# Kernel tuning notes

Hardware: AMD Instinct MI355X
Metric: run time of the kernel (lower is better)

The kernel has to match this reference:

```python
import jax, jax.numpy as jnp
import numpy as np
import math

B, W, D_IN, H = 64, 512, 300, 512

def setup_inputs() -> dict:
    key = jax.random.key(0)
    ks = jax.random.split(key, 8)
    s = 1.0 / math.sqrt(D_IN)
    return {
        "char_vectors": jax.random.normal(ks[0], (B, W, D_IN), jnp.float32),
        "word_vectors": jax.random.normal(ks[1], (B, W, D_IN), jnp.float32),
        "Wk": jax.random.uniform(ks[2], (D_IN, H), jnp.float32, -s, s),
        "bk": jnp.zeros((H,), jnp.float32),
        "Wq": jax.random.uniform(ks[3], (D_IN, H), jnp.float32, -s, s),
        "bq": jnp.zeros((H,), jnp.float32),
        "Wv": jax.random.uniform(ks[4], (D_IN, H), jnp.float32, -s, s),
        "bv": jnp.zeros((H,), jnp.float32),
    }

def reference(char_vectors, word_vectors, Wk, bk, Wq, bq, Wv, bv):
    # Stack word/char reps per word -> [B, W, 2, H]
    def proj(Wm, bm):
        return jnp.stack([word_vectors @ Wm + bm, char_vectors @ Wm + bm], axis=2)
    K = proj(Wk, bk)
    Q = proj(Wq, bq)
    V = proj(Wv, bv)
    temp = jnp.sqrt(jnp.asarray(H, jnp.float32))
    # tiny 2x2 attention per word, fully batched (dropout off = eval mode)
    attn = jnp.einsum("bwqh,bwkh->bwqk", Q, K) / temp
    attn = jax.nn.softmax(attn, axis=-1)
    out = jnp.einsum("bwqk,bwkh->bwqh", attn, V)  # [B, W, 2, H]
    return out.reshape(B, W, 2 * H)
```

## Files before the change

### kernel.cpp

```cpp
#include <hip/hip_runtime.h>

#define D 300
#define KP 328
#define KSTEPS 10
#define WPB 64
#define ROWS 128
#define NSEG 41
#define CHUNK_BYTES 41984

typedef __attribute__((ext_vector_type(4))) float f32x4;
typedef __attribute__((ext_vector_type(8))) short bf16x8;

__device__ inline unsigned short f2bf(float f) {
  unsigned int u = __float_as_uint(f);
  unsigned int r = (u + 0x7fffu + ((u >> 16) & 1u)) >> 16;
  return (unsigned short)r;
}

__device__ inline void gload_lds16(const void* g, void* l) {
  __builtin_amdgcn_global_load_lds(
      (const __attribute__((address_space(1))) unsigned int*)g,
      (__attribute__((address_space(3))) unsigned int*)l, 16, 0, 0);
}

__global__ __launch_bounds__(512) void prep_weights(
    const float* __restrict__ Wq, const float* __restrict__ Wk,
    const float* __restrict__ Wv, unsigned short* __restrict__ wt) {
  int idx = blockIdx.x * 512 + threadIdx.x;
  if (idx >= 1536 * KP) return;
  int n = idx / KP, k = idx - n * KP;
  const float* src = (n < 512) ? Wq : ((n < 1024) ? Wk : Wv);
  int col = n & 511;
  float v = (k < D) ? src[k * 512 + col] : 0.0f;
  wt[idx] = f2bf(v);
}

__device__ __forceinline__ void proj_chunk(
    const unsigned short* __restrict__ bufp, const float* __restrict__ biasL,
    int nbase, int cg, int lrow, int kgrp,
    const bf16x8 (&a)[2][KSTEPS], f32x4 (&acc)[2][2]) {
#pragma unroll
  for (int rt = 0; rt < 2; ++rt)
#pragma unroll
    for (int ct = 0; ct < 2; ++ct) {
      float b = biasL[nbase + cg * 32 + ct * 16 + lrow];
      acc[rt][ct] = (f32x4){b, b, b, b};
    }
#pragma unroll
  for (int ks = 0; ks < KSTEPS; ++ks) {
    const unsigned short* bp = bufp + cg * 32 * KP + ks * 32 + kgrp * 8;
    bf16x8 b0 = *(const bf16x8*)(bp + lrow * KP);
    bf16x8 b1 = *(const bf16x8*)(bp + (16 + lrow) * KP);
    acc[0][0] = __builtin_amdgcn_mfma_f32_16x16x32_bf16(a[0][ks], b0, acc[0][0], 0, 0, 0);
    acc[1][0] = __builtin_amdgcn_mfma_f32_16x16x32_bf16(a[1][ks], b0, acc[1][0], 0, 0, 0);
    acc[0][1] = __builtin_amdgcn_mfma_f32_16x16x32_bf16(a[0][ks], b1, acc[0][1], 0, 0, 0);
    acc[1][1] = __builtin_amdgcn_mfma_f32_16x16x32_bf16(a[1][ks], b1, acc[1][1], 0, 0, 0);
  }
}

__global__ __launch_bounds__(512, 2) void fused_attn(
    const float* __restrict__ charv, const float* __restrict__ wordv,
    const unsigned short* __restrict__ wt,
    const float* __restrict__ bk, const float* __restrict__ bq,
    const float* __restrict__ bv, float* __restrict__ out) {
  extern __shared__ char lds[];
  float* biasL = (float*)(lds + 2 * CHUNK_BYTES);
  float* sS    = biasL + 1536;
  float* sAt   = sS + 512;

  const int tid  = threadIdx.x;
  const int wid  = tid >> 6;
  const int lane = tid & 63;
  const int lrow = lane & 15;
  const int kgrp = lane >> 4;
  const int rg   = wid >> 1;
  const int cg   = wid & 1;

  auto chunk_n = [](int t) {
    return (t < 16) ? ((t & 1) * 512 + (t >> 1) * 64) : (1024 + (t - 16) * 64);
  };
  auto stage = [&](int t) {
    const char* src = (const char*)(wt + chunk_n(t) * KP);
    char* dst = lds + (t & 1) * CHUNK_BYTES;
    for (int j = wid; j < NSEG; j += 8)
      gload_lds16(src + j * 1024 + lane * 16, dst + j * 1024);
  };

  stage(0);
  for (int i = tid; i < 1536; i += 512) {
    float v = (i < 512) ? bq[i] : ((i < 1024) ? bk[i - 512] : bv[i - 1024]);
    biasL[i] = v;
  }

  bf16x8 a[2][KSTEPS];
#pragma unroll
  for (int rt = 0; rt < 2; ++rt) {
    int row = blockIdx.x * ROWS + rg * 32 + rt * 16 + lrow;
    const float* rp = ((row & 1) ? charv : wordv) + (row >> 1) * D;
#pragma unroll
    for (int ks = 0; ks < KSTEPS; ++ks) {
      int k0 = ks * 32 + kgrp * 8;
      float4 lo = {0.f, 0.f, 0.f, 0.f}, hi = {0.f, 0.f, 0.f, 0.f};
      if (k0 + 8 <= D) {
        lo = *(const float4*)(rp + k0);
        hi = *(const float4*)(rp + k0 + 4);
      } else if (k0 < D) {
        lo = *(const float4*)(rp + k0);
      }
      bf16x8 v;
      v[0] = (short)f2bf(lo.x); v[1] = (short)f2bf(lo.y);
      v[2] = (short)f2bf(lo.z); v[3] = (short)f2bf(lo.w);
      v[4] = (short)f2bf(hi.x); v[5] = (short)f2bf(hi.y);
      v[6] = (short)f2bf(hi.z); v[7] = (short)f2bf(hi.w);
      a[rt][ks] = v;
    }
  }
  __syncthreads();

  float p[2][8];
#pragma unroll
  for (int rt = 0; rt < 2; ++rt)
#pragma unroll
    for (int t = 0; t < 8; ++t) p[rt][t] = 0.f;

  int tg = 0;
  for (int g = 0; g < 8; ++g) {
    f32x4 accQ[2][2], accK[2][2];

    stage(tg + 1);
    proj_chunk((const unsigned short*)(lds + (tg & 1) * CHUNK_BYTES), biasL,
               g * 64, cg, lrow, kgrp, a, accQ);
    __syncthreads(); ++tg;

    stage(tg + 1);
    proj_chunk((const unsigned short*)(lds + (tg & 1) * CHUNK_BYTES), biasL,
               512 + g * 64, cg, lrow, kgrp, a, accK);
#pragma unroll
    for (int rt = 0; rt < 2; ++rt)
#pragma unroll
      for (int ct = 0; ct < 2; ++ct)
#pragma unroll
        for (int wl = 0; wl < 2; ++wl)
#pragma unroll
          for (int i = 0; i < 2; ++i)
#pragma unroll
            for (int j = 0; j < 2; ++j)
              p[rt][wl * 4 + i * 2 + j] += accQ[rt][ct][wl * 2 + i] * accK[rt][ct][wl * 2 + j];
    __syncthreads(); ++tg;
  }

#pragma unroll
  for (int rt = 0; rt < 2; ++rt)
#pragma unroll
    for (int t = 0; t < 8; ++t) {
      float v = p[rt][t];
      v += __shfl_xor(v, 1);
      v += __shfl_xor(v, 2);
      v += __shfl_xor(v, 4);
      v += __shfl_xor(v, 8);
      p[rt][t] = v;
    }
  if (lrow == 0) {
#pragma unroll
    for (int rt = 0; rt < 2; ++rt)
#pragma unroll
      for (int t = 0; t < 8; ++t) {
        int w = rg * 16 + rt * 8 + kgrp * 2 + (t >> 2);
        sS[cg * 256 + w * 4 + (t & 3)] = p[rt][t];
      }
  }
  __syncthreads();
  if (tid < 64) {
    const float sc = 0.044194173824159216f;
    float s[4];
#pragma unroll
    for (int t = 0; t < 4; ++t) s[t] = (sS[tid * 4 + t] + sS[256 + tid * 4 + t]) * sc;
#pragma unroll
    for (int i = 0; i < 2; ++i) {
      float m  = fmaxf(s[i * 2], s[i * 2 + 1]);
      float e0 = expf(s[i * 2] - m), e1 = expf(s[i * 2 + 1] - m);
      float inv = 1.0f / (e0 + e1);
      sAt[tid * 4 + i * 2]     = e0 * inv;
      sAt[tid * 4 + i * 2 + 1] = e1 * inv;
    }
  }
  __syncthreads();

  float at0[2][4], at1[2][4];
#pragma unroll
  for (int rt = 0; rt < 2; ++rt) {
    int wA = rg * 16 + rt * 8 + kgrp * 2;
#pragma unroll
    for (int t = 0; t < 4; ++t) {
      at0[rt][t] = sAt[wA * 4 + t];
      at1[rt][t] = sAt[(wA + 1) * 4 + t];
    }
  }

  for (int g = 0; g < 8; ++g) {
    if (tg + 1 < 24) stage(tg + 1);
    f32x4 accV[2][2];
    proj_chunk((const unsigned short*)(lds + (tg & 1) * CHUNK_BYTES), biasL,
               1024 + g * 64, cg, lrow, kgrp, a, accV);

#pragma unroll
    for (int rt = 0; rt < 2; ++rt) {
      int wA = rg * 16 + rt * 8 + kgrp * 2;
      int gA = blockIdx.x * WPB + wA;
#pragma unroll
      for (int ct = 0; ct < 2; ++ct) {
        int h = g * 64 + cg * 32 + ct * 16 + lrow;
        float* o = out + gA * 1024 + h;
        o[0]    = at0[rt][0] * accV[rt][ct][0] + at0[rt][1] * accV[rt][ct][1];
        o[512]  = at0[rt][2] * accV[rt][ct][0] + at0[rt][3] * accV[rt][ct][1];
        o[1024] = at1[rt][0] * accV[rt][ct][2] + at1[rt][1] * accV[rt][ct][3];
        o[1536] = at1[rt][2] * accV[rt][ct][2] + at1[rt][3] * accV[rt][ct][3];
      }
    }
    if (g < 7) __syncthreads();
    ++tg;
  }
}

extern "C" void kernel_launch(void* const* d_in, const int* in_sizes, int n_in,
                              void* d_out, int out_size, void* d_ws, size_t ws_size,
                              hipStream_t stream) {
  const float* charv = (const float*)d_in[0];
  const float* wordv = (const float*)d_in[1];
  const float* Wk = (const float*)d_in[2];
  const float* bk = (const float*)d_in[3];
  const float* Wq = (const float*)d_in[4];
  const float* bq = (const float*)d_in[5];
  const float* Wv = (const float*)d_in[6];
  const float* bv = (const float*)d_in[7];
  float* out = (float*)d_out;
  unsigned short* wt = (unsigned short*)d_ws;

  prep_weights<<<(1536 * KP + 511) / 512, 512, 0, stream>>>(Wq, Wk, Wv, wt);

  const int lds_bytes = 2 * CHUNK_BYTES + 1536 * 4 + 512 * 4 + 256 * 4;
  fused_attn<<<32768 / WPB, 512, lds_bytes, stream>>>(charv, wordv, wt, bk, bq, bv, out);
}
```

Before: 98.16 us.

## Double rows per block and interleave Q/K halves into one staged chunk

Each block now handles 256 rows (128 words) instead of 128, so every staged weight chunk in LDS is reused across four row tiles per wave. That halves total weight traffic from L2 and the barrier count per row. The Q/K phase now stages 32 Q columns and their matching 32 K columns together in one chunk, cutting that phase to 16 pipelined steps with no Q-then-K barrier in between. The A-fragment registers double to 4x10 bf16x8, which raises VGPR pressure under launch_bounds(512,2). The grid drops to 256 blocks, which may underfill the GPU's CUs.

Measured after the change: 126.0 us. +28.4%, slower.

```diff
diff --git a/kernel.cpp b/kernel.cpp
--- a/kernel.cpp
+++ b/kernel.cpp
@@ -3,10 +3,12 @@
 #define D 300
 #define KP 328
 #define KSTEPS 10
-#define WPB 64
-#define ROWS 128
+#define WPB 128
+#define ROWS 256
 #define NSEG 41
 #define CHUNK_BYTES 41984
+#define HALF_BYTES 20992
+#define NCHUNK 24
 
 typedef __attribute__((ext_vector_type(4))) float f32x4;
 typedef __attribute__((ext_vector_type(8))) short bf16x8;
@@ -35,29 +37,6 @@
   wt[idx] = f2bf(v);
 }
 
-__device__ __forceinline__ void proj_chunk(
-    const unsigned short* __restrict__ bufp, const float* __restrict__ biasL,
-    int nbase, int cg, int lrow, int kgrp,
-    const bf16x8 (&a)[2][KSTEPS], f32x4 (&acc)[2][2]) {
-#pragma unroll
-  for (int rt = 0; rt < 2; ++rt)
-#pragma unroll
-    for (int ct = 0; ct < 2; ++ct) {
-      float b = biasL[nbase + cg * 32 + ct * 16 + lrow];
-      acc[rt][ct] = (f32x4){b, b, b, b};
-    }
-#pragma unroll
-  for (int ks = 0; ks < KSTEPS; ++ks) {
-    const unsigned short* bp = bufp + cg * 32 * KP + ks * 32 + kgrp * 8;
-    bf16x8 b0 = *(const bf16x8*)(bp + lrow * KP);
-    bf16x8 b1 = *(const bf16x8*)(bp + (16 + lrow) * KP);
-    acc[0][0] = __builtin_amdgcn_mfma_f32_16x16x32_bf16(a[0][ks], b0, acc[0][0], 0, 0, 0);
-    acc[1][0] = __builtin_amdgcn_mfma_f32_16x16x32_bf16(a[1][ks], b0, acc[1][0], 0, 0, 0);
-    acc[0][1] = __builtin_amdgcn_mfma_f32_16x16x32_bf16(a[0][ks], b1, acc[0][1], 0, 0, 0);
-    acc[1][1] = __builtin_amdgcn_mfma_f32_16x16x32_bf16(a[1][ks], b1, acc[1][1], 0, 0, 0);
-  }
-}
-
 __global__ __launch_bounds__(512, 2) void fused_attn(
     const float* __restrict__ charv, const float* __restrict__ wordv,
     const unsigned short* __restrict__ wt,
@@ -66,7 +45,7 @@
   extern __shared__ char lds[];
   float* biasL = (float*)(lds + 2 * CHUNK_BYTES);
   float* sS    = biasL + 1536;
-  float* sAt   = sS + 512;
+  float* sAt   = sS + 1024;
 
   const int tid  = threadIdx.x;
   const int wid  = tid >> 6;
@@ -76,14 +55,25 @@
   const int rg   = wid >> 1;
   const int cg   = wid & 1;
 
-  auto chunk_n = [](int t) {
-    return (t < 16) ? ((t & 1) * 512 + (t >> 1) * 64) : (1024 + (t - 16) * 64);
-  };
   auto stage = [&](int t) {
-    const char* src = (const char*)(wt + chunk_n(t) * KP);
+    const char* p0;
+    const char* p1;
+    int split;
+    if (t < 16) {
+      p0 = (const char*)(wt + t * 32 * KP);
+      p1 = (const char*)(wt + (512 + t * 32) * KP) - HALF_BYTES;
+      split = HALF_BYTES;
+    } else {
+      p0 = (const char*)(wt + (1024 + (t - 16) * 64) * KP);
+      p1 = p0;
+      split = 1 << 30;
+    }
     char* dst = lds + (t & 1) * CHUNK_BYTES;
-    for (int j = wid; j < NSEG; j += 8)
-      gload_lds16(src + j * 1024 + lane * 16, dst + j * 1024);
+    for (int j = wid; j < NSEG; j += 8) {
+      int b = j * 1024 + lane * 16;
+      const char* src = (b < split) ? p0 : p1;
+      gload_lds16(src + b, dst + j * 1024);
+    }
   };
 
   stage(0);
@@ -92,10 +82,10 @@
     biasL[i] = v;
   }
 
-  bf16x8 a[2][KSTEPS];
-#pragma unroll
-  for (int rt = 0; rt < 2; ++rt) {
-    int row = blockIdx.x * ROWS + rg * 32 + rt * 16 + lrow;
+  bf16x8 a[4][KSTEPS];
+#pragma unroll
+  for (int rt = 0; rt < 4; ++rt) {
+    int row = blockIdx.x * ROWS + rg * 64 + rt * 16 + lrow;
     const float* rp = ((row & 1) ? charv : wordv) + (row >> 1) * D;
 #pragma unroll
     for (int ks = 0; ks < KSTEPS; ++ks) {
@@ -117,40 +107,48 @@
   }
   __syncthreads();
 
-  float p[2][8];
-#pragma unroll
-  for (int rt = 0; rt < 2; ++rt)
+  float p[4][8];
+#pragma unroll
+  for (int rt = 0; rt < 4; ++rt)
 #pragma unroll
     for (int t = 0; t < 8; ++t) p[rt][t] = 0.f;
 
-  int tg = 0;
-  for (int g = 0; g < 8; ++g) {
-    f32x4 accQ[2][2], accK[2][2];
-
-    stage(tg + 1);
-    proj_chunk((const unsigned short*)(lds + (tg & 1) * CHUNK_BYTES), biasL,
-               g * 64, cg, lrow, kgrp, a, accQ);
-    __syncthreads(); ++tg;
-
-    stage(tg + 1);
-    proj_chunk((const unsigned short*)(lds + (tg & 1) * CHUNK_BYTES), biasL,
-               512 + g * 64, cg, lrow, kgrp, a, accK);
-#pragma unroll
-    for (int rt = 0; rt < 2; ++rt)
-#pragma unroll
-      for (int ct = 0; ct < 2; ++ct)
-#pragma unroll
-        for (int wl = 0; wl < 2; ++wl)
-#pragma unroll
-          for (int i = 0; i < 2; ++i)
-#pragma unroll
-            for (int j = 0; j < 2; ++j)
-              p[rt][wl * 4 + i * 2 + j] += accQ[rt][ct][wl * 2 + i] * accK[rt][ct][wl * 2 + j];
-    __syncthreads(); ++tg;
-  }
-
-#pragma unroll
-  for (int rt = 0; rt < 2; ++rt)
+  for (int t = 0; t < 16; ++t) {
+    stage(t + 1);
+    const unsigned short* bufp = (const unsigned short*)(lds + (t & 1) * CHUNK_BYTES);
+    float bqv = biasL[t * 32 + cg * 16 + lrow];
+    float bkv = biasL[512 + t * 32 + cg * 16 + lrow];
+    f32x4 accQ[4], accK[4];
+#pragma unroll
+    for (int rt = 0; rt < 4; ++rt) {
+      accQ[rt] = (f32x4){bqv, bqv, bqv, bqv};
+      accK[rt] = (f32x4){bkv, bkv, bkv, bkv};
+    }
+    const unsigned short* pq = bufp + (cg * 16 + lrow) * KP + kgrp * 8;
+#pragma unroll
+    for (int ks = 0; ks < KSTEPS; ++ks) {
+      bf16x8 b0 = *(const bf16x8*)(pq + ks * 32);
+      bf16x8 b1 = *(const bf16x8*)(pq + 32 * KP + ks * 32);
+#pragma unroll
+      for (int rt = 0; rt < 4; ++rt) {
+        accQ[rt] = __builtin_amdgcn_mfma_f32_16x16x32_bf16(a[rt][ks], b0, accQ[rt], 0, 0, 0);
+        accK[rt] = __builtin_amdgcn_mfma_f32_16x16x32_bf16(a[rt][ks], b1, accK[rt], 0, 0, 0);
+      }
+    }
+#pragma unroll
+    for (int rt = 0; rt < 4; ++rt)
+#pragma unroll
+      for (int wl = 0; wl < 2; ++wl)
+#pragma unroll
+        for (int i = 0; i < 2; ++i)
+#pragma unroll
+          for (int j = 0; j < 2; ++j)
+            p[rt][wl * 4 + i * 2 + j] += accQ[rt][wl * 2 + i] * accK[rt][wl * 2 + j];
+    __syncthreads();
+  }
+
+#pragma unroll
+  for (int rt = 0; rt < 4; ++rt)
 #pragma unroll
     for (int t = 0; t < 8; ++t) {
       float v = p[rt][t];
@@ -162,19 +160,19 @@
     }
   if (lrow == 0) {
 #pragma unroll
-    for (int rt = 0; rt < 2; ++rt)
+    for (int rt = 0; rt < 4; ++rt)
 #pragma unroll
       for (int t = 0; t < 8; ++t) {
-        int w = rg * 16 + rt * 8 + kgrp * 2 + (t >> 2);
-        sS[cg * 256 + w * 4 + (t & 3)] = p[rt][t];
+        int w = rg * 32 + rt * 8 + kgrp * 2 + (t >> 2);
+        sS[cg * 512 + w * 4 + (t & 3)] = p[rt][t];
       }
   }
   __syncthreads();
-  if (tid < 64) {
+  if (tid < 128) {
     const float sc = 0.044194173824159216f;
     float s[4];
 #pragma unroll
-    for (int t = 0; t < 4; ++t) s[t] = (sS[tid * 4 + t] + sS[256 + tid * 4 + t]) * sc;
+    for (int t = 0; t < 4; ++t) s[t] = (sS[tid * 4 + t] + sS[512 + tid * 4 + t]) * sc;
 #pragma unroll
     for (int i = 0; i < 2; ++i) {
       float m  = fmaxf(s[i * 2], s[i * 2 + 1]);
@@ -186,10 +184,10 @@
   }
   __syncthreads();
 
-  float at0[2][4], at1[2][4];
-#pragma unroll
-  for (int rt = 0; rt < 2; ++rt) {
-    int wA = rg * 16 + rt * 8 + kgrp * 2;
+  float at0[4][4], at1[4][4];
+#pragma unroll
+  for (int rt = 0; rt < 4; ++rt) {
+    int wA = rg * 32 + rt * 8 + kgrp * 2;
 #pragma unroll
     for (int t = 0; t < 4; ++t) {
       at0[rt][t] = sAt[wA * 4 + t];
@@ -197,16 +195,31 @@
     }
   }
 
-  for (int g = 0; g < 8; ++g) {
-    if (tg + 1 < 24) stage(tg + 1);
-    f32x4 accV[2][2];
-    proj_chunk((const unsigned short*)(lds + (tg & 1) * CHUNK_BYTES), biasL,
-               1024 + g * 64, cg, lrow, kgrp, a, accV);
-
-#pragma unroll
-    for (int rt = 0; rt < 2; ++rt) {
-      int wA = rg * 16 + rt * 8 + kgrp * 2;
-      int gA = blockIdx.x * WPB + wA;
+  for (int t = 16; t < 24; ++t) {
+    if (t + 1 < 24) stage(t + 1);
+    const unsigned short* bufp = (const unsigned short*)(lds + (t & 1) * CHUNK_BYTES);
+    const int g = t - 16;
+    f32x4 accV[4][2];
+#pragma unroll
+    for (int ct = 0; ct < 2; ++ct) {
+      float b = biasL[1024 + g * 64 + cg * 32 + ct * 16 + lrow];
+#pragma unroll
+      for (int rt = 0; rt < 4; ++rt) accV[rt][ct] = (f32x4){b, b, b, b};
+    }
+    const unsigned short* pv = bufp + (cg * 32 + lrow) * KP + kgrp * 8;
+#pragma unroll
+    for (int ks = 0; ks < KSTEPS; ++ks) {
+      bf16x8 b0 = *(const bf16x8*)(pv + ks * 32);
+      bf16x8 b1 = *(const bf16x8*)(pv + 16 * KP + ks * 32);
+#pragma unroll
+      for (int rt = 0; rt < 4; ++rt) {
+        accV[rt][0] = __builtin_amdgcn_mfma_f32_16x16x32_bf16(a[rt][ks], b0, accV[rt][0], 0, 0, 0);
+        accV[rt][1] = __builtin_amdgcn_mfma_f32_16x16x32_bf16(a[rt][ks], b1, accV[rt][1], 0, 0, 0);
+      }
+    }
+#pragma unroll
+    for (int rt = 0; rt < 4; ++rt) {
+      int gA = blockIdx.x * WPB + rg * 32 + rt * 8 + kgrp * 2;
 #pragma unroll
       for (int ct = 0; ct < 2; ++ct) {
         int h = g * 64 + cg * 32 + ct * 16 + lrow;
@@ -217,8 +230,7 @@
         o[1536] = at1[rt][2] * accV[rt][ct][2] + at1[rt][3] * accV[rt][ct][3];
       }
     }
-    if (g < 7) __syncthreads();
-    ++tg;
+    if (t + 1 < 24) __syncthreads();
   }
 }
 
@@ -238,6 +250,6 @@
 
   prep_weights<<<(1536 * KP + 511) / 512, 512, 0, stream>>>(Wq, Wk, Wv, wt);
 
-  const int lds_bytes = 2 * CHUNK_BYTES + 1536 * 4 + 512 * 4 + 256 * 4;
-  fused_attn<<<32768 / WPB, 512, lds_bytes, stream>>>(charv, wordv, wt, bk, bq, bv, out);
-}
+  const int lds_bytes = 2 * CHUNK_BYTES + 1536 * 4 + 1024 * 4 + 512 * 4;
+  fused_attn<<<65536 / ROWS, 512, lds_bytes, stream>>>(charv, wordv, wt, bk, bq, bv, out);
+}
```

## Triple-buffer weight chunks with fragment-ordered layout and fused Q/K chunks

Applied to the files above, without the earlier changes.

Weights are repacked into 24 contiguous chunks in MFMA-fragment order, with Q and K columns interleaved so each chunk carries both. The kernel now uses a three-buffer LDS ring with two chunks in flight, synchronised by explicit vmcnt and lgkmcnt waits plus raw barriers in place of __syncthreads. The aim is to hide global-to-LDS latency better and to remove padded strided LDS reads. In exchange, LDS use grows, the occupancy hint of 2 blocks per CU is dropped, and correctness depends on hand-tuned wait counts.

After: 98.64 us. Within noise of the previous version (+0.5%).

```diff
diff --git a/kernel.cpp b/kernel.cpp
--- a/kernel.cpp
+++ b/kernel.cpp
@@ -1,12 +1,14 @@
 #include <hip/hip_runtime.h>
 
 #define D 300
-#define KP 328
+#define HDIM 512
+#define ROWS 128
+#define WPB 64
 #define KSTEPS 10
-#define WPB 64
-#define ROWS 128
-#define NSEG 41
-#define CHUNK_BYTES 41984
+#define NCH 24
+#define CH_BYTES 40960
+#define CH_ELEMS 20480
+#define SEGW 5
 
 typedef __attribute__((ext_vector_type(4))) float f32x4;
 typedef __attribute__((ext_vector_type(8))) short bf16x8;
@@ -27,46 +29,28 @@
     const float* __restrict__ Wq, const float* __restrict__ Wk,
     const float* __restrict__ Wv, unsigned short* __restrict__ wt) {
   int idx = blockIdx.x * 512 + threadIdx.x;
-  if (idx >= 1536 * KP) return;
-  int n = idx / KP, k = idx - n * KP;
-  const float* src = (n < 512) ? Wq : ((n < 1024) ? Wk : Wv);
-  int col = n & 511;
-  float v = (k < D) ? src[k * 512 + col] : 0.0f;
+  int c = idx / CH_ELEMS, r = idx - c * CH_ELEMS;
+  int ks = r >> 11, r2 = r & 2047;
+  int col = r2 >> 5, kk = r2 & 31;
+  int k = ks * 32 + kk;
+  const float* M; int gcol;
+  if (c < 16) {
+    if (col < 32) { M = Wq; gcol = c * 32 + col; }
+    else          { M = Wk; gcol = c * 32 + col - 32; }
+  } else { M = Wv; gcol = (c - 16) * 64 + col; }
+  float v = (k < D) ? M[k * HDIM + gcol] : 0.0f;
   wt[idx] = f2bf(v);
 }
 
-__device__ __forceinline__ void proj_chunk(
-    const unsigned short* __restrict__ bufp, const float* __restrict__ biasL,
-    int nbase, int cg, int lrow, int kgrp,
-    const bf16x8 (&a)[2][KSTEPS], f32x4 (&acc)[2][2]) {
-#pragma unroll
-  for (int rt = 0; rt < 2; ++rt)
-#pragma unroll
-    for (int ct = 0; ct < 2; ++ct) {
-      float b = biasL[nbase + cg * 32 + ct * 16 + lrow];
-      acc[rt][ct] = (f32x4){b, b, b, b};
-    }
-#pragma unroll
-  for (int ks = 0; ks < KSTEPS; ++ks) {
-    const unsigned short* bp = bufp + cg * 32 * KP + ks * 32 + kgrp * 8;
-    bf16x8 b0 = *(const bf16x8*)(bp + lrow * KP);
-    bf16x8 b1 = *(const bf16x8*)(bp + (16 + lrow) * KP);
-    acc[0][0] = __builtin_amdgcn_mfma_f32_16x16x32_bf16(a[0][ks], b0, acc[0][0], 0, 0, 0);
-    acc[1][0] = __builtin_amdgcn_mfma_f32_16x16x32_bf16(a[1][ks], b0, acc[1][0], 0, 0, 0);
-    acc[0][1] = __builtin_amdgcn_mfma_f32_16x16x32_bf16(a[0][ks], b1, acc[0][1], 0, 0, 0);
-    acc[1][1] = __builtin_amdgcn_mfma_f32_16x16x32_bf16(a[1][ks], b1, acc[1][1], 0, 0, 0);
-  }
-}
-
-__global__ __launch_bounds__(512, 2) void fused_attn(
+__global__ __launch_bounds__(512) void fused_attn(
     const float* __restrict__ charv, const float* __restrict__ wordv,
     const unsigned short* __restrict__ wt,
     const float* __restrict__ bk, const float* __restrict__ bq,
     const float* __restrict__ bv, float* __restrict__ out) {
   extern __shared__ char lds[];
-  float* biasL = (float*)(lds + 2 * CHUNK_BYTES);
+  float* biasL = (float*)(lds + 3 * CH_BYTES);
   float* sS    = biasL + 1536;
-  float* sAt   = sS + 512;
+  float* sAt   = sS;
 
   const int tid  = threadIdx.x;
   const int wid  = tid >> 6;
@@ -76,22 +60,18 @@
   const int rg   = wid >> 1;
   const int cg   = wid & 1;
 
-  auto chunk_n = [](int t) {
-    return (t < 16) ? ((t & 1) * 512 + (t >> 1) * 64) : (1024 + (t - 16) * 64);
+  auto stage = [&](int t) {
+    const char* src = (const char*)wt + (long)t * CH_BYTES + wid * (SEGW * 1024) + lane * 16;
+    char* dst = lds + (t % 3) * CH_BYTES + wid * (SEGW * 1024);
+#pragma unroll
+    for (int j = 0; j < SEGW; ++j)
+      gload_lds16(src + j * 1024, dst + j * 1024);
   };
-  auto stage = [&](int t) {
-    const char* src = (const char*)(wt + chunk_n(t) * KP);
-    char* dst = lds + (t & 1) * CHUNK_BYTES;
-    for (int j = wid; j < NSEG; j += 8)
-      gload_lds16(src + j * 1024 + lane * 16, dst + j * 1024);
-  };
-
-  stage(0);
+
   for (int i = tid; i < 1536; i += 512) {
     float v = (i < 512) ? bq[i] : ((i < 1024) ? bk[i - 512] : bv[i - 1024]);
     biasL[i] = v;
   }
-
   bf16x8 a[2][KSTEPS];
 #pragma unroll
   for (int rt = 0; rt < 2; ++rt) {
@@ -115,7 +95,8 @@
       a[rt][ks] = v;
     }
   }
-  __syncthreads();
+  stage(0);
+  stage(1);
 
   float p[2][8];
 #pragma unroll
@@ -123,30 +104,37 @@
 #pragma unroll
     for (int t = 0; t < 8; ++t) p[rt][t] = 0.f;
 
-  int tg = 0;
-  for (int g = 0; g < 8; ++g) {
-    f32x4 accQ[2][2], accK[2][2];
-
-    stage(tg + 1);
-    proj_chunk((const unsigned short*)(lds + (tg & 1) * CHUNK_BYTES), biasL,
-               g * 64, cg, lrow, kgrp, a, accQ);
-    __syncthreads(); ++tg;
-
-    stage(tg + 1);
-    proj_chunk((const unsigned short*)(lds + (tg & 1) * CHUNK_BYTES), biasL,
-               512 + g * 64, cg, lrow, kgrp, a, accK);
+  const int fq = (cg * 16 + lrow) * 64 + kgrp * 16;
+
+  for (int t = 0; t < 16; ++t) {
+    asm volatile("s_waitcnt vmcnt(5)" ::: "memory");
+    asm volatile("s_waitcnt lgkmcnt(0)" ::: "memory");
+    __builtin_amdgcn_s_barrier();
+    stage(t + 2);
+    const char* buf = lds + (t % 3) * CH_BYTES;
+    float bqv = biasL[t * 32 + cg * 16 + lrow];
+    float bkv = biasL[512 + t * 32 + cg * 16 + lrow];
+    f32x4 accQ[2], accK[2];
+    accQ[0] = (f32x4){bqv, bqv, bqv, bqv}; accQ[1] = accQ[0];
+    accK[0] = (f32x4){bkv, bkv, bkv, bkv}; accK[1] = accK[0];
+#pragma unroll
+    for (int ks = 0; ks < KSTEPS; ++ks) {
+      bf16x8 bquf = *(const bf16x8*)(buf + ks * 4096 + fq);
+      bf16x8 bkuf = *(const bf16x8*)(buf + ks * 4096 + fq + 2048);
+      accQ[0] = __builtin_amdgcn_mfma_f32_16x16x32_bf16(a[0][ks], bquf, accQ[0], 0, 0, 0);
+      accQ[1] = __builtin_amdgcn_mfma_f32_16x16x32_bf16(a[1][ks], bquf, accQ[1], 0, 0, 0);
+      accK[0] = __builtin_amdgcn_mfma_f32_16x16x32_bf16(a[0][ks], bkuf, accK[0], 0, 0, 0);
+      accK[1] = __builtin_amdgcn_mfma_f32_16x16x32_bf16(a[1][ks], bkuf, accK[1], 0, 0, 0);
+    }
 #pragma unroll
     for (int rt = 0; rt < 2; ++rt)
 #pragma unroll
-      for (int ct = 0; ct < 2; ++ct)
-#pragma unroll
-        for (int wl = 0; wl < 2; ++wl)
-#pragma unroll
-          for (int i = 0; i < 2; ++i)
-#pragma unroll
-            for (int j = 0; j < 2; ++j)
-              p[rt][wl * 4 + i * 2 + j] += accQ[rt][ct][wl * 2 + i] * accK[rt][ct][wl * 2 + j];
-    __syncthreads(); ++tg;
+      for (int wl = 0; wl < 2; ++wl)
+#pragma unroll
+        for (int i = 0; i < 2; ++i)
+#pragma unroll
+          for (int j = 0; j < 2; ++j)
+            p[rt][wl * 4 + i * 2 + j] += accQ[rt][wl * 2 + i] * accK[rt][wl * 2 + j];
   }
 
 #pragma unroll
@@ -169,7 +157,8 @@
         sS[cg * 256 + w * 4 + (t & 3)] = p[rt][t];
       }
   }
-  __syncthreads();
+  asm volatile("s_waitcnt lgkmcnt(0)" ::: "memory");
+  __builtin_amdgcn_s_barrier();
   if (tid < 64) {
     const float sc = 0.044194173824159216f;
     float s[4];
@@ -184,7 +173,8 @@
       sAt[tid * 4 + i * 2 + 1] = e1 * inv;
     }
   }
-  __syncthreads();
+  asm volatile("s_waitcnt lgkmcnt(0)" ::: "memory");
+  __builtin_amdgcn_s_barrier();
 
   float at0[2][4], at1[2][4];
 #pragma unroll
@@ -197,16 +187,34 @@
     }
   }
 
-  for (int g = 0; g < 8; ++g) {
-    if (tg + 1 < 24) stage(tg + 1);
+  for (int t = 16; t < NCH; ++t) {
+    if (t == 16) asm volatile("s_waitcnt vmcnt(5)" ::: "memory");
+    else         asm volatile("s_waitcnt vmcnt(21)" ::: "memory");
+    asm volatile("s_waitcnt lgkmcnt(0)" ::: "memory");
+    __builtin_amdgcn_s_barrier();
+    if (t + 2 < NCH) stage(t + 2);
+    const char* buf = lds + (t % 3) * CH_BYTES;
+    const int g = t - 16;
     f32x4 accV[2][2];
-    proj_chunk((const unsigned short*)(lds + (tg & 1) * CHUNK_BYTES), biasL,
-               1024 + g * 64, cg, lrow, kgrp, a, accV);
-
+#pragma unroll
+    for (int ct = 0; ct < 2; ++ct) {
+      float b = biasL[1024 + g * 64 + cg * 32 + ct * 16 + lrow];
+      accV[0][ct] = (f32x4){b, b, b, b};
+      accV[1][ct] = accV[0][ct];
+    }
+    const int fv = (cg * 32 + lrow) * 64 + kgrp * 16;
+#pragma unroll
+    for (int ks = 0; ks < KSTEPS; ++ks) {
+      bf16x8 b0 = *(const bf16x8*)(buf + ks * 4096 + fv);
+      bf16x8 b1 = *(const bf16x8*)(buf + ks * 4096 + fv + 1024);
+      accV[0][0] = __builtin_amdgcn_mfma_f32_16x16x32_bf16(a[0][ks], b0, accV[0][0], 0, 0, 0);
+      accV[1][0] = __builtin_amdgcn_mfma_f32_16x16x32_bf16(a[1][ks], b0, accV[1][0], 0, 0, 0);
+      accV[0][1] = __builtin_amdgcn_mfma_f32_16x16x32_bf16(a[0][ks], b1, accV[0][1], 0, 0, 0);
+      accV[1][1] = __builtin_amdgcn_mfma_f32_16x16x32_bf16(a[1][ks], b1, accV[1][1], 0, 0, 0);
+    }
 #pragma unroll
     for (int rt = 0; rt < 2; ++rt) {
-      int wA = rg * 16 + rt * 8 + kgrp * 2;
-      int gA = blockIdx.x * WPB + wA;
+      int gA = blockIdx.x * WPB + rg * 16 + rt * 8 + kgrp * 2;
 #pragma unroll
       for (int ct = 0; ct < 2; ++ct) {
         int h = g * 64 + cg * 32 + ct * 16 + lrow;
@@ -217,8 +225,6 @@
         o[1536] = at1[rt][2] * accV[rt][ct][2] + at1[rt][3] * accV[rt][ct][3];
       }
     }
-    if (g < 7) __syncthreads();
-    ++tg;
   }
 }
 
@@ -236,8 +242,8 @@
   float* out = (float*)d_out;
   unsigned short* wt = (unsigned short*)d_ws;
 
-  prep_weights<<<(1536 * KP + 511) / 512, 512, 0, stream>>>(Wq, Wk, Wv, wt);
-
-  const int lds_bytes = 2 * CHUNK_BYTES + 1536 * 4 + 512 * 4 + 256 * 4;
-  fused_attn<<<32768 / WPB, 512, lds_bytes, stream>>>(charv, wordv, wt, bk, bq, bv, out);
-}
+  prep_weights<<<NCH * CH_ELEMS / 512, 512, 0, stream>>>(Wq, Wk, Wv, wt);
+
+  const int lds_bytes = 3 * CH_BYTES + 1536 * 4 + 512 * 4;
+  fused_attn<<<65536 / ROWS, 512, lds_bytes, stream>>>(charv, wordv, wt, bk, bq, bv, out);
+}
```
